# Kernel tuning notes

Hardware: AMD Instinct MI355X
Metric: run time of the kernel (lower is better)

Reference implementation:

```python
import jax, jax.numpy as jnp
import numpy as np

DIM = 1024
N_HEADS = 16
HEAD_DIM = 64


def setup_inputs() -> dict:
    key = jax.random.key(0)
    kx, kq, kk, kv, ko = jax.random.split(key, 5)
    B, T = 4, 2048
    s = DIM ** -0.5  # roughly torch Linear init scale
    return {
        "x": jax.random.normal(kx, (B, T, DIM), dtype=jnp.float32),
        "Wq": jax.random.normal(kq, (DIM, DIM), dtype=jnp.float32) * s,
        "Wk": jax.random.normal(kk, (DIM, DIM), dtype=jnp.float32) * s,
        "Wv": jax.random.normal(kv, (DIM, DIM), dtype=jnp.float32) * s,
        "Wo": jax.random.normal(ko, (DIM, DIM), dtype=jnp.float32) * s,
    }


def reference(x, Wq, Wk, Wv, Wo):
    B, T, D = x.shape
    h, hd = N_HEADS, HEAD_DIM
    # torch nn.Linear: y = x @ W.T
    q = (x @ Wq.T).reshape(B, T, h, hd).transpose(0, 2, 1, 3)  # [B,h,T,hd]
    k = (x @ Wk.T).reshape(B, T, h, hd).transpose(0, 2, 1, 3)
    v = (x @ Wv.T).reshape(B, T, h, hd).transpose(0, 2, 1, 3)
    scale = hd ** -0.5
    # The torch loop over query chunks with full-K softmax is mathematically
    # identical to full (non-causal) softmax attention.
    scores = jnp.einsum("bhqd,bhkd->bhqk", q, k) * scale  # [B,h,T,T]
    attn = jax.nn.softmax(scores, axis=-1)
    out = jnp.einsum("bhqk,bhkd->bhqd", attn, v)  # [B,h,T,hd]
    out = out.transpose(0, 2, 1, 3).reshape(B, T, D)
    return out @ Wo.T
```

## Files before the change

kernel.cpp:

```cpp
#include <hip/hip_runtime.h>

typedef float f32x4 __attribute__((ext_vector_type(4)));
typedef float f32x16 __attribute__((ext_vector_type(16)));
typedef short s16x8 __attribute__((ext_vector_type(8)));
typedef unsigned int u32x4 __attribute__((ext_vector_type(4)));

#define B_SZ 4
#define T_SZ 2048
#define D_SZ 1024
#define NH 16
#define HD 64
#define KVB 256

#define CLQ (0.125f * 1.44269504089f)

__device__ __forceinline__ unsigned short f2b(float f) {
  unsigned int u = __builtin_bit_cast(unsigned int, f);
  unsigned int r = (u + 0x7fffu + ((u >> 16) & 1u)) >> 16;
  return (unsigned short)r;
}

__device__ __forceinline__ void gld_lds16(void* lds, const void* g) {
  __builtin_amdgcn_global_load_lds(
      (const __attribute__((address_space(1))) unsigned int*)g,
      (__attribute__((address_space(3))) unsigned int*)lds, 16, 0, 0);
}

__device__ __forceinline__ float vsum16(f32x16 v) {
  float t0 = (v[0] + v[1]) + (v[2] + v[3]);
  float t1 = (v[4] + v[5]) + (v[6] + v[7]);
  float t2 = (v[8] + v[9]) + (v[10] + v[11]);
  float t3 = (v[12] + v[13]) + (v[14] + v[15]);
  return (t0 + t1) + (t2 + t3);
}

__global__ void cast_all(const float* __restrict__ x,
                         const float* __restrict__ w0, const float* __restrict__ w1,
                         const float* __restrict__ w2, const float* __restrict__ w3,
                         unsigned short* __restrict__ xo,
                         unsigned short* __restrict__ o0, unsigned short* __restrict__ o1,
                         unsigned short* __restrict__ o2, unsigned short* __restrict__ o3) {
  int i = blockIdx.x * blockDim.x + threadIdx.x;
  const float* src;
  unsigned short* dst;
  int j;
  if (i < 2097152) {
    src = x; dst = xo; j = i;
  } else {
    const int t = i - 2097152;
    const int w = t >> 18;
    j = t & 262143;
    src = (w == 0) ? w0 : (w == 1) ? w1 : (w == 2) ? w2 : w3;
    dst = (w == 0) ? o0 : (w == 1) ? o1 : (w == 2) ? o2 : o3;
  }
  float4 v = reinterpret_cast<const float4*>(src)[j];
  ushort4 o;
  o.x = f2b(v.x); o.y = f2b(v.y); o.z = f2b(v.z); o.w = f2b(v.w);
  reinterpret_cast<ushort4*>(dst)[j] = o;
}

#define BM 128
#define BN 128
#define BKG 64

__global__ __launch_bounds__(256, 2) void gemm_qkv(
    const unsigned short* __restrict__ A,
    const unsigned short* __restrict__ Wq,
    const unsigned short* __restrict__ Wk,
    const unsigned short* __restrict__ Wv,
    unsigned short* __restrict__ Qo,
    unsigned short* __restrict__ Ko,
    unsigned short* __restrict__ Vto) {
  __shared__ __align__(16) char As[BM * 128];
  __shared__ __align__(16) char Ws[BN * 128];
  const int tid = threadIdx.x, wid = tid >> 6, lane = tid & 63;
  const int sel = blockIdx.y >> 3;
  const unsigned short* W = (sel == 0) ? Wq : (sel == 1) ? Wk : Wv;
  const int row0 = blockIdx.x * BM, col0 = (blockIdx.y & 7) * BN;
  const int wr = (wid >> 1) * 64, wc = (wid & 1) * 64;
  const int fr = lane & 15;
  const int kgB = (lane >> 4) * 16;
  f32x4 acc[4][4] = {};

  const int srow = lane >> 3;
  const int sc = lane & 7;
  const int sch = sc ^ srow;

  for (int k0 = 0; k0 < D_SZ; k0 += BKG) {
    __syncthreads();
#pragma unroll
    for (int i = 0; i < 4; ++i) {
      const int c = wid + 4 * i;
      const int row = c * 8 + srow;
      gld_lds16(As + c * 1024, &A[(row0 + row) * D_SZ + k0 + sch * 8]);
      gld_lds16(Ws + c * 1024, &W[(col0 + row) * D_SZ + k0 + sch * 8]);
    }
    __syncthreads();
    s16x8 af[4][2], bf[4][2];
#pragma unroll
    for (int m = 0; m < 4; ++m) {
      const int row = wr + m * 16 + fr;
#pragma unroll
      for (int kk = 0; kk < 2; ++kk)
        af[m][kk] = *(const s16x8*)(As + row * 128 + ((kk * 64 + kgB) ^ ((row & 7) << 4)));
    }
#pragma unroll
    for (int n = 0; n < 4; ++n) {
      const int row = wc + n * 16 + fr;
#pragma unroll
      for (int kk = 0; kk < 2; ++kk)
        bf[n][kk] = *(const s16x8*)(Ws + row * 128 + ((kk * 64 + kgB) ^ ((row & 7) << 4)));
    }
#pragma unroll
    for (int kk = 0; kk < 2; ++kk)
#pragma unroll
      for (int m = 0; m < 4; ++m)
#pragma unroll
        for (int n = 0; n < 4; ++n)
          acc[m][n] = __builtin_amdgcn_mfma_f32_16x16x32_bf16(af[m][kk], bf[n][kk], acc[m][n], 0, 0, 0);
  }

  const int crow = row0 + wr + ((lane >> 4) << 2);
  const int ccol = col0 + wc + fr;
  if (sel == 2) {
#pragma unroll
    for (int m = 0; m < 4; ++m)
#pragma unroll
      for (int n = 0; n < 4; ++n) {
        ushort4 pk;
        pk.x = f2b(acc[m][n][0]); pk.y = f2b(acc[m][n][1]);
        pk.z = f2b(acc[m][n][2]); pk.w = f2b(acc[m][n][3]);
        const int tok = crow + m * 16;
        const int c = ccol + n * 16;
        *(ushort4*)&Vto[((tok >> 11) * 1024 + c) * 2048 + (tok & 2047)] = pk;
      }
  } else {
    unsigned short* C = (sel == 0) ? Qo : Ko;
    const float s = (sel == 0) ? CLQ : 1.0f;
#pragma unroll
    for (int m = 0; m < 4; ++m)
#pragma unroll
      for (int n = 0; n < 4; ++n)
#pragma unroll
        for (int r = 0; r < 4; ++r)
          C[(crow + m * 16 + r) * D_SZ + ccol + n * 16] = f2b(acc[m][n][r] * s);
  }
}

__global__ __launch_bounds__(256, 2) void gemm_out(
    const unsigned short* __restrict__ A,
    const unsigned short* __restrict__ W,
    float* __restrict__ C, int M, int N, int K) {
  __shared__ __align__(16) char As[BM * 128];
  __shared__ __align__(16) char Ws[BN * 128];
  const int tid = threadIdx.x, wid = tid >> 6, lane = tid & 63;
  const int row0 = blockIdx.x * BM, col0 = blockIdx.y * BN;
  const int wr = (wid >> 1) * 64, wc = (wid & 1) * 64;
  const int fr = lane & 15;
  const int kgB = (lane >> 4) * 16;
  f32x4 acc[4][4] = {};

  const int srow = lane >> 3;
  const int sc = lane & 7;
  const int sch = sc ^ srow;

  for (int k0 = 0; k0 < K; k0 += BKG) {
    __syncthreads();
#pragma unroll
    for (int i = 0; i < 4; ++i) {
      const int c = wid + 4 * i;
      const int row = c * 8 + srow;
      gld_lds16(As + c * 1024, &A[(row0 + row) * K + k0 + sch * 8]);
      gld_lds16(Ws + c * 1024, &W[(col0 + row) * K + k0 + sch * 8]);
    }
    __syncthreads();
    s16x8 af[4][2], bf[4][2];
#pragma unroll
    for (int m = 0; m < 4; ++m) {
      const int row = wr + m * 16 + fr;
#pragma unroll
      for (int kk = 0; kk < 2; ++kk)
        af[m][kk] = *(const s16x8*)(As + row * 128 + ((kk * 64 + kgB) ^ ((row & 7) << 4)));
    }
#pragma unroll
    for (int n = 0; n < 4; ++n) {
      const int row = wc + n * 16 + fr;
#pragma unroll
      for (int kk = 0; kk < 2; ++kk)
        bf[n][kk] = *(const s16x8*)(Ws + row * 128 + ((kk * 64 + kgB) ^ ((row & 7) << 4)));
    }
#pragma unroll
    for (int kk = 0; kk < 2; ++kk)
#pragma unroll
      for (int m = 0; m < 4; ++m)
#pragma unroll
        for (int n = 0; n < 4; ++n)
          acc[m][n] = __builtin_amdgcn_mfma_f32_16x16x32_bf16(af[m][kk], bf[n][kk], acc[m][n], 0, 0, 0);
  }

  const int crow = row0 + wr + ((lane >> 4) << 2);
  const int ccol = col0 + wc + fr;
#pragma unroll
  for (int m = 0; m < 4; ++m)
#pragma unroll
    for (int n = 0; n < 4; ++n)
#pragma unroll
      for (int r = 0; r < 4; ++r)
        C[(crow + m * 16 + r) * N + ccol + n * 16] = acc[m][n][r];
}

__global__ __launch_bounds__(256, 2) void attn_kernel(
    const unsigned short* __restrict__ Q,
    const unsigned short* __restrict__ K,
    const unsigned short* __restrict__ Vt,
    unsigned short* __restrict__ O) {
  __shared__ __align__(16) char Kl[KVB * 128];
  __shared__ __align__(16) char Vl[HD * 512];

  const int tid = threadIdx.x, wid = tid >> 6, lane = tid & 63;
  const int ql = lane & 31;
  const int hi = lane >> 5;
  const int srow = lane >> 3;
  const int sc = lane & 7;
  const int vrow = lane >> 5;
  const int vsc = lane & 31;

  const int lin = blockIdx.y * gridDim.x + blockIdx.x;
  const int work = (lin & 7) * 64 + (lin >> 3);
  const int qc = work & 7, bh = work >> 3;
  const int b = bh >> 4, h = bh & 15;
  const int q0 = qc * 256 + wid * 64;
  const int qkbase = b * T_SZ * D_SZ + h * HD;
  const int vtbase = (b * D_SZ + h * HD) * T_SZ;

  s16x8 qf[2][4];
#pragma unroll
  for (int c = 0; c < 2; ++c)
#pragma unroll
    for (int kq = 0; kq < 4; ++kq)
      qf[c][kq] = *(const s16x8*)&Q[qkbase + (q0 + c * 32 + ql) * D_SZ + kq * 16 + hi * 8];

  f32x16 ot[2][2] = {};
  float l[2] = {0.f, 0.f};

#pragma unroll 1
  for (int kv0 = 0; kv0 < T_SZ; kv0 += KVB) {
    __syncthreads();
#pragma unroll
    for (int i = 0; i < 8; ++i) {
      const int c = wid + 4 * i;
      const int row = c * 8 + srow;
      const int sch = sc ^ (row & 7);
      gld_lds16(Kl + c * 1024, &K[qkbase + (kv0 + row) * D_SZ + sch * 8]);
    }
#pragma unroll
    for (int i = 0; i < 8; ++i) {
      const int c = wid + 4 * i;
      const int row = c * 2 + vrow;
      const int sslot = vsc ^ (row & 7);
      gld_lds16(Vl + c * 1024, &Vt[vtbase + row * T_SZ + kv0 + sslot * 8]);
    }
    __syncthreads();

#pragma unroll 1
    for (int sub = 0; sub < 4; ++sub) {
      s16x8 vfr[4][2];
#pragma unroll
      for (int ks = 0; ks < 4; ++ks)
#pragma unroll
        for (int dblk = 0; dblk < 2; ++dblk) {
          const int vr = dblk * 32 + ql;
          vfr[ks][dblk] = *(const s16x8*)(Vl + vr * 512 +
                            ((sub * 128 + ks * 32 + hi * 16) ^ ((vr & 7) << 4)));
        }

      f32x16 st[2][2] = {};
#pragma unroll
      for (int blk = 0; blk < 2; ++blk)
#pragma unroll
        for (int kq = 0; kq < 4; ++kq) {
          const int kr = sub * 64 + blk * 32 + ql;
          const s16x8 k8 = *(const s16x8*)(Kl + kr * 128 +
                             ((kq * 32 + hi * 16) ^ ((kr & 7) << 4)));
#pragma unroll
          for (int c = 0; c < 2; ++c)
            st[c][blk] = __builtin_amdgcn_mfma_f32_32x32x16_bf16(k8, qf[c][kq], st[c][blk], 0, 0, 0);
        }

#pragma unroll
      for (int c = 0; c < 2; ++c) {
#pragma unroll
        for (int blk = 0; blk < 2; ++blk)
#pragma unroll
          for (int r = 0; r < 16; ++r)
            st[c][blk][r] = __builtin_amdgcn_exp2f(st[c][blk][r]);
        l[c] += vsum16(st[c][0]) + vsum16(st[c][1]);
      }

#pragma unroll
      for (int c = 0; c < 2; ++c) {
        s16x8 pf[4];
#pragma unroll
        for (int ks = 0; ks < 4; ++ks) {
          const int blk = ks >> 1, rb = (ks & 1) * 8;
          unsigned int a0, a1, b0, b1;
          asm("v_cvt_pk_bf16_f32 %0, %1, %2" : "=v"(a0) : "v"(st[c][blk][rb + 0]), "v"(st[c][blk][rb + 1]));
          asm("v_cvt_pk_bf16_f32 %0, %1, %2" : "=v"(a1) : "v"(st[c][blk][rb + 2]), "v"(st[c][blk][rb + 3]));
          asm("v_cvt_pk_bf16_f32 %0, %1, %2" : "=v"(b0) : "v"(st[c][blk][rb + 4]), "v"(st[c][blk][rb + 5]));
          asm("v_cvt_pk_bf16_f32 %0, %1, %2" : "=v"(b1) : "v"(st[c][blk][rb + 6]), "v"(st[c][blk][rb + 7]));
          asm("v_permlane32_swap_b32 %0, %1" : "+v"(a0), "+v"(b0));
          asm("v_permlane32_swap_b32 %0, %1" : "+v"(a1), "+v"(b1));
          u32x4 w = {a0, a1, b0, b1};
          pf[ks] = __builtin_bit_cast(s16x8, w);
        }
#pragma unroll
        for (int ks = 0; ks < 4; ++ks)
#pragma unroll
          for (int dblk = 0; dblk < 2; ++dblk)
            ot[c][dblk] = __builtin_amdgcn_mfma_f32_32x32x16_bf16(vfr[ks][dblk], pf[ks], ot[c][dblk], 0, 0, 0);
      }
    }
  }

#pragma unroll
  for (int c = 0; c < 2; ++c) {
    const float lt = l[c] + __shfl_xor(l[c], 32, 64);
    const float inv = 1.f / lt;
    const int orow = qkbase + (q0 + c * 32 + ql) * D_SZ;
#pragma unroll
    for (int dblk = 0; dblk < 2; ++dblk)
#pragma unroll
      for (int qd = 0; qd < 4; ++qd) {
        ushort4 pk;
        pk.x = f2b(ot[c][dblk][qd * 4 + 0] * inv);
        pk.y = f2b(ot[c][dblk][qd * 4 + 1] * inv);
        pk.z = f2b(ot[c][dblk][qd * 4 + 2] * inv);
        pk.w = f2b(ot[c][dblk][qd * 4 + 3] * inv);
        *(ushort4*)&O[orow + dblk * 32 + qd * 8 + hi * 4] = pk;
      }
  }
}

extern "C" void kernel_launch(void* const* d_in, const int* in_sizes, int n_in,
                              void* d_out, int out_size, void* d_ws, size_t ws_size,
                              hipStream_t stream) {
  const float* x  = (const float*)d_in[0];
  const float* Wq = (const float*)d_in[1];
  const float* Wk = (const float*)d_in[2];
  const float* Wv = (const float*)d_in[3];
  const float* Wo = (const float*)d_in[4];

  const int NTOK = B_SZ * T_SZ;
  const int SZX = NTOK * D_SZ;
  const int SZW = D_SZ * D_SZ;

  unsigned short* ws  = (unsigned short*)d_ws;
  unsigned short* xb  = ws;
  unsigned short* wqb = xb + SZX;
  unsigned short* wkb = wqb + SZW;
  unsigned short* wvb = wkb + SZW;
  unsigned short* wob = wvb + SZW;
  unsigned short* Qb  = wob + SZW;
  unsigned short* Kb  = Qb + SZX;
  unsigned short* Vtb = Kb + SZX;

  cast_all<<<(2097152 + 4 * 262144) / 256, 256, 0, stream>>>(
      x, Wq, Wk, Wv, Wo, xb, wqb, wkb, wvb, wob);

  dim3 gq(NTOK / BM, 24);
  gemm_qkv<<<gq, 256, 0, stream>>>(xb, wqb, wkb, wvb, Qb, Kb, Vtb);

  dim3 ga(T_SZ / 256, B_SZ * NH);
  attn_kernel<<<ga, 256, 0, stream>>>(Qb, Kb, Vtb, xb);

  dim3 gg(NTOK / BM, D_SZ / BN);
  gemm_out<<<gg, 256, 0, stream>>>(xb, wob, (float*)d_out, NTOK, D_SZ, D_SZ);
}
```

Before: 161.7 us.

## Double GEMM K-tile to 128 and remap blocks across XCDs for L2 locality

Both projection GEMMs now stage a 128-wide K slice per iteration, so LDS per block doubles and there are half as many barrier pairs per K loop. The load mapping and XOR swizzle are adapted to the 256-byte LDS rows, and the inner compute runs as a non-unrolled loop over four 32-wide sub-steps. Block indices are remapped so consecutive blocks on the same XCD share row tiles, aiming for better L2 reuse. The larger LDS footprint (64 KB per block) may reduce occupancy below the two blocks per CU requested in launch bounds.

Measured after the change: 166.7 us. +3.1%, slower.

```diff
diff --git a/kernel.cpp b/kernel.cpp
--- a/kernel.cpp
+++ b/kernel.cpp
@@ -61,7 +61,7 @@
 
 #define BM 128
 #define BN 128
-#define BKG 64
+#define BKG 128
 
 __global__ __launch_bounds__(256, 2) void gemm_qkv(
     const unsigned short* __restrict__ A,
@@ -71,53 +71,56 @@
     unsigned short* __restrict__ Qo,
     unsigned short* __restrict__ Ko,
     unsigned short* __restrict__ Vto) {
-  __shared__ __align__(16) char As[BM * 128];
-  __shared__ __align__(16) char Ws[BN * 128];
+  __shared__ __align__(16) char As[BM * 256];
+  __shared__ __align__(16) char Ws[BN * 256];
   const int tid = threadIdx.x, wid = tid >> 6, lane = tid & 63;
-  const int sel = blockIdx.y >> 3;
+
+  const int lin = blockIdx.y * gridDim.x + blockIdx.x;
+  const int xcd = lin & 7, t = lin >> 3;
+  const int wx = xcd * 8 + (t & 7);
+  const int wy = t >> 3;
+  const int sel = wy >> 3;
   const unsigned short* W = (sel == 0) ? Wq : (sel == 1) ? Wk : Wv;
-  const int row0 = blockIdx.x * BM, col0 = (blockIdx.y & 7) * BN;
+  const int row0 = wx * BM, col0 = (wy & 7) * BN;
+
   const int wr = (wid >> 1) * 64, wc = (wid & 1) * 64;
   const int fr = lane & 15;
   const int kgB = (lane >> 4) * 16;
   f32x4 acc[4][4] = {};
 
-  const int srow = lane >> 3;
-  const int sc = lane & 7;
-  const int sch = sc ^ srow;
+  const int srow = lane >> 4;
+  const int s16 = lane & 15;
 
   for (int k0 = 0; k0 < D_SZ; k0 += BKG) {
     __syncthreads();
 #pragma unroll
-    for (int i = 0; i < 4; ++i) {
+    for (int i = 0; i < 8; ++i) {
       const int c = wid + 4 * i;
-      const int row = c * 8 + srow;
-      gld_lds16(As + c * 1024, &A[(row0 + row) * D_SZ + k0 + sch * 8]);
-      gld_lds16(Ws + c * 1024, &W[(col0 + row) * D_SZ + k0 + sch * 8]);
-    }
-    __syncthreads();
-    s16x8 af[4][2], bf[4][2];
-#pragma unroll
-    for (int m = 0; m < 4; ++m) {
-      const int row = wr + m * 16 + fr;
-#pragma unroll
-      for (int kk = 0; kk < 2; ++kk)
-        af[m][kk] = *(const s16x8*)(As + row * 128 + ((kk * 64 + kgB) ^ ((row & 7) << 4)));
-    }
-#pragma unroll
-    for (int n = 0; n < 4; ++n) {
-      const int row = wc + n * 16 + fr;
-#pragma unroll
-      for (int kk = 0; kk < 2; ++kk)
-        bf[n][kk] = *(const s16x8*)(Ws + row * 128 + ((kk * 64 + kgB) ^ ((row & 7) << 4)));
-    }
-#pragma unroll
-    for (int kk = 0; kk < 2; ++kk)
+      const int row = c * 4 + srow;
+      const int ss = s16 ^ (row & 7);
+      gld_lds16(As + c * 1024, &A[(row0 + row) * D_SZ + k0 + ss * 8]);
+      gld_lds16(Ws + c * 1024, &W[(col0 + row) * D_SZ + k0 + ss * 8]);
+    }
+    __syncthreads();
+#pragma unroll 1
+    for (int kks = 0; kks < 4; ++kks) {
+      s16x8 af[4], bf[4];
+#pragma unroll
+      for (int m = 0; m < 4; ++m) {
+        const int row = wr + m * 16 + fr;
+        af[m] = *(const s16x8*)(As + row * 256 + ((kks * 64 + kgB) ^ ((row & 7) << 4)));
+      }
+#pragma unroll
+      for (int n = 0; n < 4; ++n) {
+        const int row = wc + n * 16 + fr;
+        bf[n] = *(const s16x8*)(Ws + row * 256 + ((kks * 64 + kgB) ^ ((row & 7) << 4)));
+      }
 #pragma unroll
       for (int m = 0; m < 4; ++m)
 #pragma unroll
         for (int n = 0; n < 4; ++n)
-          acc[m][n] = __builtin_amdgcn_mfma_f32_16x16x32_bf16(af[m][kk], bf[n][kk], acc[m][n], 0, 0, 0);
+          acc[m][n] = __builtin_amdgcn_mfma_f32_16x16x32_bf16(af[m], bf[n], acc[m][n], 0, 0, 0);
+    }
   }
 
   const int crow = row0 + wr + ((lane >> 4) << 2);
@@ -151,51 +154,54 @@
     const unsigned short* __restrict__ A,
     const unsigned short* __restrict__ W,
     float* __restrict__ C, int M, int N, int K) {
-  __shared__ __align__(16) char As[BM * 128];
-  __shared__ __align__(16) char Ws[BN * 128];
+  __shared__ __align__(16) char As[BM * 256];
+  __shared__ __align__(16) char Ws[BN * 256];
   const int tid = threadIdx.x, wid = tid >> 6, lane = tid & 63;
-  const int row0 = blockIdx.x * BM, col0 = blockIdx.y * BN;
+
+  const int lin = blockIdx.y * gridDim.x + blockIdx.x;
+  const int xcd = lin & 7, t = lin >> 3;
+  const int wx = xcd * 8 + (t & 7);
+  const int wy = t >> 3;
+  const int row0 = wx * BM, col0 = wy * BN;
+
   const int wr = (wid >> 1) * 64, wc = (wid & 1) * 64;
   const int fr = lane & 15;
   const int kgB = (lane >> 4) * 16;
   f32x4 acc[4][4] = {};
 
-  const int srow = lane >> 3;
-  const int sc = lane & 7;
-  const int sch = sc ^ srow;
+  const int srow = lane >> 4;
+  const int s16 = lane & 15;
 
   for (int k0 = 0; k0 < K; k0 += BKG) {
     __syncthreads();
 #pragma unroll
-    for (int i = 0; i < 4; ++i) {
+    for (int i = 0; i < 8; ++i) {
       const int c = wid + 4 * i;
-      const int row = c * 8 + srow;
-      gld_lds16(As + c * 1024, &A[(row0 + row) * K + k0 + sch * 8]);
-      gld_lds16(Ws + c * 1024, &W[(col0 + row) * K + k0 + sch * 8]);
-    }
-    __syncthreads();
-    s16x8 af[4][2], bf[4][2];
-#pragma unroll
-    for (int m = 0; m < 4; ++m) {
-      const int row = wr + m * 16 + fr;
-#pragma unroll
-      for (int kk = 0; kk < 2; ++kk)
-        af[m][kk] = *(const s16x8*)(As + row * 128 + ((kk * 64 + kgB) ^ ((row & 7) << 4)));
-    }
-#pragma unroll
-    for (int n = 0; n < 4; ++n) {
-      const int row = wc + n * 16 + fr;
-#pragma unroll
-      for (int kk = 0; kk < 2; ++kk)
-        bf[n][kk] = *(const s16x8*)(Ws + row * 128 + ((kk * 64 + kgB) ^ ((row & 7) << 4)));
-    }
-#pragma unroll
-    for (int kk = 0; kk < 2; ++kk)
+      const int row = c * 4 + srow;
+      const int ss = s16 ^ (row & 7);
+      gld_lds16(As + c * 1024, &A[(row0 + row) * K + k0 + ss * 8]);
+      gld_lds16(Ws + c * 1024, &W[(col0 + row) * K + k0 + ss * 8]);
+    }
+    __syncthreads();
+#pragma unroll 1
+    for (int kks = 0; kks < 4; ++kks) {
+      s16x8 af[4], bf[4];
+#pragma unroll
+      for (int m = 0; m < 4; ++m) {
+        const int row = wr + m * 16 + fr;
+        af[m] = *(const s16x8*)(As + row * 256 + ((kks * 64 + kgB) ^ ((row & 7) << 4)));
+      }
+#pragma unroll
+      for (int n = 0; n < 4; ++n) {
+        const int row = wc + n * 16 + fr;
+        bf[n] = *(const s16x8*)(Ws + row * 256 + ((kks * 64 + kgB) ^ ((row & 7) << 4)));
+      }
 #pragma unroll
       for (int m = 0; m < 4; ++m)
 #pragma unroll
         for (int n = 0; n < 4; ++n)
-          acc[m][n] = __builtin_amdgcn_mfma_f32_16x16x32_bf16(af[m][kk], bf[n][kk], acc[m][n], 0, 0, 0);
+          acc[m][n] = __builtin_amdgcn_mfma_f32_16x16x32_bf16(af[m], bf[n], acc[m][n], 0, 0, 0);
+    }
   }
 
   const int crow = row0 + wr + ((lane >> 4) << 2);
```
